# Kernel tuning notes

Hardware: AMD Instinct MI355X
Metric: run time of the kernel (lower is better)

## Reference

```python
import jax, jax.numpy as jnp
import numpy as np

D = 1024
H = 16
DH = D // H
FF = 4096
EPS = 1e-6


def setup_inputs() -> dict:
    key = jax.random.key(0)
    ks = jax.random.split(key, 8)
    s = 1.0 / np.sqrt(D)
    return {
        "x": jax.random.normal(ks[0], (2, 2048, D), jnp.float32),
        # attention projections stored [in, out] (math equals torch Linear x @ W.T)
        "w_q": jax.random.normal(ks[1], (D, D), jnp.float32) * s,
        "w_k": jax.random.normal(ks[2], (D, D), jnp.float32) * s,
        "w_v": jax.random.normal(ks[3], (D, D), jnp.float32) * s,
        "w_o": jax.random.normal(ks[4], (D, D), jnp.float32) * s,
        "w1": jax.random.normal(ks[5], (D, FF), jnp.float32) * s,
        "b1": jnp.zeros((FF,), jnp.float32),
        "w2": jax.random.normal(ks[6], (FF, D), jnp.float32) * (1.0 / np.sqrt(FF)),
        "b2": jnp.zeros((D,), jnp.float32),
        "g1": jnp.ones((D,), jnp.float32),
        "be1": jnp.zeros((D,), jnp.float32),
        "g2": jnp.ones((D,), jnp.float32),
        "be2": jnp.zeros((D,), jnp.float32),
    }


def _layernorm(x, gamma, beta):
    # torch .std() uses Bessel correction (ddof=1); note std+eps, not var+eps
    mean = jnp.mean(x, axis=-1, keepdims=True)
    std = jnp.std(x, axis=-1, keepdims=True, ddof=1)
    return gamma * (x - mean) / (std + EPS) + beta


def _attention(h, w_q, w_k, w_v, w_o):
    B, S, _ = h.shape
    q = (h @ w_q).reshape(B, S, H, DH)
    k = (h @ w_k).reshape(B, S, H, DH)
    v = (h @ w_v).reshape(B, S, H, DH)
    scores = jnp.einsum('bqhd,bkhd->bhqk', q, k) / np.sqrt(DH)  # [B,H,S,S]
    attn = jax.nn.softmax(scores, axis=-1)
    out = jnp.einsum('bhqk,bkhd->bqhd', attn, v).reshape(B, S, D)
    return out @ w_o


def reference(x, w_q, w_k, w_v, w_o, w1, b1, w2, b2, g1, be1, g2, be2):
    # pre-norm residual 1: self-attention (dropout=0 / eval)
    x = x + _attention(_layernorm(x, g1, be1), w_q, w_k, w_v, w_o)
    # pre-norm residual 2: FFN
    h = _layernorm(x, g2, be2)
    x = x + (jax.nn.relu(h @ w1 + b1) @ w2 + b2)
    return x
```

## Files before the change

### kernel.cpp

```cpp
#include <hip/hip_runtime.h>


typedef _Float16 half8 __attribute__((ext_vector_type(8)));
typedef _Float16 half4 __attribute__((ext_vector_type(4)));
typedef float floatx4 __attribute__((ext_vector_type(4)));

__device__ __forceinline__ void async16(const void* g, void* l) {
    __builtin_amdgcn_global_load_lds((const __attribute__((address_space(1))) unsigned int*)g,
                                     (__attribute__((address_space(3))) unsigned int*)l,
                                     16, 0, 0);
}

__global__ __launch_bounds__(256) void ln_kernel(const float* __restrict__ x,
                                                 const float* __restrict__ g,
                                                 const float* __restrict__ be,
                                                 _Float16* __restrict__ out) {
    int row = blockIdx.x;
    int tid = threadIdx.x;
    floatx4 v = ((const floatx4*)(x + (size_t)row * 1024))[tid];
    float s = 0.f, ss = 0.f;
#pragma unroll
    for (int i = 0; i < 4; i++) { s += v[i]; ss += v[i] * v[i]; }
#pragma unroll
    for (int off = 1; off < 64; off <<= 1) {
        s += __shfl_xor(s, off);
        ss += __shfl_xor(ss, off);
    }
    __shared__ float sm[8];
    int wave = tid >> 6, lane = tid & 63;
    if (lane == 0) { sm[wave] = s; sm[wave + 4] = ss; }
    __syncthreads();
    s = sm[0] + sm[1] + sm[2] + sm[3];
    ss = sm[4] + sm[5] + sm[6] + sm[7];
    float mean = s * (1.f / 1024.f);
    float var = (ss - s * mean) * (1.f / 1023.f);
    float rs = 1.f / (sqrtf(fmaxf(var, 0.f)) + 1e-6f);
    floatx4 gv = ((const floatx4*)g)[tid];
    floatx4 bv = ((const floatx4*)be)[tid];
    half4 o;
#pragma unroll
    for (int i = 0; i < 4; i++) o[i] = (_Float16)(gv[i] * (v[i] - mean) * rs + bv[i]);
    ((half4*)(out + (size_t)row * 1024))[tid] = o;
}

__global__ __launch_bounds__(256) void convt_kernel(const float* __restrict__ W, int ldW,
                                                    _Float16* __restrict__ WT, int Kr) {
    __shared__ float t[64][65];
    int n0 = blockIdx.x * 64, k0 = blockIdx.y * 64;
    int tid = threadIdx.x;
    int r = tid >> 4, c4 = (tid & 15) * 4;
#pragma unroll
    for (int p = 0; p < 4; p++) {
        floatx4 v = *(const floatx4*)(W + (size_t)(k0 + r + p * 16) * ldW + n0 + c4);
#pragma unroll
        for (int j = 0; j < 4; j++) t[c4 + j][r + p * 16] = v[j];
    }
    __syncthreads();
#pragma unroll
    for (int p = 0; p < 4; p++) {
        int rr = r + p * 16;
        half4 o;
#pragma unroll
        for (int j = 0; j < 4; j++) o[j] = (_Float16)t[rr][c4 + j];
        *(half4*)(WT + (size_t)(n0 + rr) * Kr + k0 + c4) = o;
    }
}

__global__ __launch_bounds__(256) void transv_kernel(const _Float16* __restrict__ V,
                                                     _Float16* __restrict__ Vt) {
    __shared__ _Float16 t[64][72];
    int t0 = blockIdx.x * 64, d0 = blockIdx.y * 64;
    int tid = threadIdx.x;
#pragma unroll
    for (int i = 0; i < 2; i++) {
        int v = tid + i * 256;
        int r = v >> 3, c = (v & 7) * 8;
        half8 vv = *(const half8*)(V + (size_t)(t0 + r) * 1024 + d0 + c);
#pragma unroll
        for (int j = 0; j < 8; j++) t[c + j][r] = vv[j];
    }
    __syncthreads();
    int bh = (t0 >> 11) * 16 + (d0 >> 6);
    int sbase = t0 & 2047;
#pragma unroll
    for (int i = 0; i < 2; i++) {
        int v = tid + i * 256;
        int r = v >> 3, c = (v & 7) * 8;
        half8 o = *(const half8*)&t[r][c];
        *(half8*)(Vt + ((size_t)bh * 64 + r) * 2048 + sbase + c) = o;
    }
}

__global__ __launch_bounds__(256) void gemm_t(const _Float16* __restrict__ A,
                                              const _Float16* __restrict__ BT,
                                              const float* __restrict__ bias,
                                              const float* res, void* Cout,
                                              int N, int K, int relu_flag, int out_fp16) {
    __shared__ _Float16 As[64 * 64];
    __shared__ _Float16 Bs[128 * 64];
    int tid = threadIdx.x;
    int wave = tid >> 6, lane = tid & 63, quad = lane >> 4, l15 = lane & 15;
    int bm = blockIdx.y * 64, bn = blockIdx.x * 128;
    int wr = (wave & 1) * 32, wc = (wave >> 1) * 64;
    int lrow = lane >> 3, lch = lane & 7;

    floatx4 acc[2][4];
#pragma unroll
    for (int im = 0; im < 2; im++)
#pragma unroll
        for (int in = 0; in < 4; in++)
#pragma unroll
            for (int r = 0; r < 4; r++) acc[im][in][r] = 0.f;

    for (int k0 = 0; k0 < K; k0 += 64) {
        __syncthreads();
#pragma unroll
        for (int ia = 0; ia < 2; ia++) {
            int gidx = 2 * wave + ia;
            int row = gidx * 8 + lrow;
            int ch = lch ^ (row & 7);
            async16(A + (size_t)(bm + row) * K + k0 + ch * 8, &As[gidx * 512]);
        }
#pragma unroll
        for (int ib = 0; ib < 4; ib++) {
            int gidx = 4 * wave + ib;
            int row = gidx * 8 + lrow;
            int ch = lch ^ (row & 7);
            async16(BT + (size_t)(bn + row) * K + k0 + ch * 8, &Bs[gidx * 512]);
        }
        __syncthreads();

        half8 af[2][2], bf[4][2];
#pragma unroll
        for (int kk = 0; kk < 2; kk++) {
#pragma unroll
            for (int im = 0; im < 2; im++) {
                int m = wr + im * 16 + l15;
                af[im][kk] = *(const half8*)&As[m * 64 + ((((kk << 2) | quad) ^ (m & 7)) << 3)];
            }
#pragma unroll
            for (int in = 0; in < 4; in++) {
                int n = wc + in * 16 + l15;
                bf[in][kk] = *(const half8*)&Bs[n * 64 + ((((kk << 2) | quad) ^ (n & 7)) << 3)];
            }
        }
#pragma unroll
        for (int kk = 0; kk < 2; kk++)
#pragma unroll
            for (int im = 0; im < 2; im++)
#pragma unroll
                for (int in = 0; in < 4; in++)
                    acc[im][in] = __builtin_amdgcn_mfma_f32_16x16x32_f16(af[im][kk], bf[in][kk],
                                                                         acc[im][in], 0, 0, 0);
    }
#pragma unroll
    for (int im = 0; im < 2; im++)
#pragma unroll
        for (int in = 0; in < 4; in++)
#pragma unroll
            for (int r = 0; r < 4; r++) {
                int row = bm + wr + im * 16 + quad * 4 + r;
                int col = bn + wc + in * 16 + l15;
                float val = acc[im][in][r];
                if (bias) val += bias[col];
                if (relu_flag) val = fmaxf(val, 0.f);
                if (res) val += res[(size_t)row * N + col];
                if (out_fp16) ((_Float16*)Cout)[(size_t)row * N + col] = (_Float16)val;
                else          ((float*)Cout)[(size_t)row * N + col] = val;
            }
}

__global__ __launch_bounds__(256) void attn_kernel(const _Float16* Q,
                                                   const _Float16* __restrict__ K,
                                                   const _Float16* __restrict__ Vt,
                                                   _Float16* O) {
    __shared__ _Float16 Qs[64 * 64];
    __shared__ _Float16 Ks[64 * 64];
    __shared__ _Float16 Vs[64 * 64];
    int qt = blockIdx.x, bh = blockIdx.y;
    int b = bh >> 4, h = bh & 15;
    int col0 = h * 64, tbase = b * 2048;
    int tid = threadIdx.x;
    int wave = tid >> 6, lane = tid & 63, quad = lane >> 4, l15 = lane & 15;
    int lrow = lane >> 3, lch = lane & 7;

#pragma unroll
    for (int i = 0; i < 2; i++) {
        int g = 2 * wave + i;
        int row = g * 8 + lrow;
        int ch = lch ^ (row & 7);
        async16(Q + (size_t)(tbase + qt * 64 + row) * 1024 + col0 + ch * 8, &Qs[g * 512]);
    }

    floatx4 o_acc[4];
#pragma unroll
    for (int im = 0; im < 4; im++)
#pragma unroll
        for (int r = 0; r < 4; r++) o_acc[im][r] = 0.f;
    float m_i = -1e30f, l_i = 0.f;

    for (int kt = 0; kt < 32; kt++) {
        __syncthreads();
#pragma unroll
        for (int i = 0; i < 2; i++) {
            int g = 2 * wave + i;
            int row = g * 8 + lrow;
            int ch = lch ^ (row & 7);
            async16(K + (size_t)(tbase + kt * 64 + row) * 1024 + col0 + ch * 8, &Ks[g * 512]);
            async16(Vt + ((size_t)bh * 64 + row) * 2048 + kt * 64 + ch * 8, &Vs[g * 512]);
        }
        __syncthreads();

        int rowq = 16 * wave + l15;
        half8 bq[2];
#pragma unroll
        for (int kk = 0; kk < 2; kk++)
            bq[kk] = *(const half8*)&Qs[rowq * 64 + ((((kk << 2) | quad) ^ (rowq & 7)) << 3)];
        floatx4 s_acc[4];
#pragma unroll
        for (int jn = 0; jn < 4; jn++)
#pragma unroll
            for (int r = 0; r < 4; r++) s_acc[jn][r] = 0.f;
#pragma unroll
        for (int jn = 0; jn < 4; jn++) {
            int rowk = 16 * jn + l15;
#pragma unroll
            for (int kk = 0; kk < 2; kk++) {
                half8 ak = *(const half8*)&Ks[rowk * 64 + ((((kk << 2) | quad) ^ (rowk & 7)) << 3)];
                s_acc[jn] = __builtin_amdgcn_mfma_f32_16x16x32_f16(ak, bq[kk], s_acc[jn], 0, 0, 0);
            }
        }

        float mx = -1e30f;
#pragma unroll
        for (int jn = 0; jn < 4; jn++)
#pragma unroll
            for (int r = 0; r < 4; r++) {
                s_acc[jn][r] *= 0.125f;
                mx = fmaxf(mx, s_acc[jn][r]);
            }
        mx = fmaxf(mx, __shfl_xor(mx, 16));
        mx = fmaxf(mx, __shfl_xor(mx, 32));
        float mnew = fmaxf(m_i, mx);
        float dd = m_i - mnew;
        float alpha = (dd < -60.f) ? 0.f : __expf(dd);
        m_i = mnew;

        float sum = 0.f;
#pragma unroll
        for (int jn = 0; jn < 4; jn++)
#pragma unroll
            for (int r = 0; r < 4; r++) {
                float d2 = s_acc[jn][r] - mnew;
                float p = (d2 < -60.f) ? 0.f : __expf(d2);
                s_acc[jn][r] = p;
                sum += p;
            }
        sum += __shfl_xor(sum, 16);
        sum += __shfl_xor(sum, 32);
        l_i = l_i * alpha + sum;

        half4 pb[4];
#pragma unroll
        for (int jn = 0; jn < 4; jn++)
#pragma unroll
            for (int r = 0; r < 4; r++) pb[jn][r] = (_Float16)s_acc[jn][r];

#pragma unroll
        for (int im = 0; im < 4; im++)
#pragma unroll
            for (int r = 0; r < 4; r++) o_acc[im][r] *= alpha;
#pragma unroll
        for (int im = 0; im < 4; im++) {
            int rowv = 16 * im + l15;
#pragma unroll
            for (int ks = 0; ks < 4; ks++) {
                int off = rowv * 128 + ((((2 * ks) | (quad >> 1)) ^ (rowv & 7)) << 4) + (quad & 1) * 8;
                half4 av = *(const half4*)((const char*)Vs + off);
                o_acc[im] = __builtin_amdgcn_mfma_f32_16x16x16f16(av, pb[ks], o_acc[im], 0, 0, 0);
            }
        }
    }

    float rl = 1.f / l_i;
#pragma unroll
    for (int im = 0; im < 4; im++) {
        half4 o;
#pragma unroll
        for (int r = 0; r < 4; r++) o[r] = (_Float16)(o_acc[im][r] * rl);
        *(half4*)&O[(size_t)(tbase + qt * 64 + wave * 16 + l15) * 1024 + col0 + im * 16 + quad * 4] = o;
    }
}

extern "C" void kernel_launch(void* const* d_in, const int* in_sizes, int n_in,
                              void* d_out, int out_size, void* d_ws, size_t ws_size,
                              hipStream_t stream) {
    const float* x   = (const float*)d_in[0];
    const float* wq  = (const float*)d_in[1];
    const float* wk  = (const float*)d_in[2];
    const float* wv  = (const float*)d_in[3];
    const float* wo  = (const float*)d_in[4];
    const float* w1  = (const float*)d_in[5];
    const float* b1  = (const float*)d_in[6];
    const float* w2  = (const float*)d_in[7];
    const float* b2  = (const float*)d_in[8];
    const float* g1  = (const float*)d_in[9];
    const float* be1 = (const float*)d_in[10];
    const float* g2  = (const float*)d_in[11];
    const float* be2 = (const float*)d_in[12];

    const size_t M1 = (size_t)1 << 20;
    _Float16* R0 = (_Float16*)d_ws;
    _Float16* R1 = R0 + 4 * M1;
    _Float16* R2 = R0 + 8 * M1;
    _Float16* R3 = R0 + 12 * M1;

    _Float16* wqT = (_Float16*)d_out;
    _Float16* wkT = wqT + 1 * M1;
    _Float16* wvT = wqT + 2 * M1;
    float* x1 = (float*)d_out;
    float* out = (float*)d_out;

    dim3 blk(256);

    convt_kernel<<<dim3(16, 16), blk, 0, stream>>>(wq, 1024, wqT, 1024);
    convt_kernel<<<dim3(16, 16), blk, 0, stream>>>(wk, 1024, wkT, 1024);
    convt_kernel<<<dim3(16, 16), blk, 0, stream>>>(wv, 1024, wvT, 1024);
    ln_kernel<<<4096, blk, 0, stream>>>(x, g1, be1, R0);
    gemm_t<<<dim3(8, 64), blk, 0, stream>>>(R0, wqT, nullptr, nullptr, R1, 1024, 1024, 0, 1);
    gemm_t<<<dim3(8, 64), blk, 0, stream>>>(R0, wkT, nullptr, nullptr, R2, 1024, 1024, 0, 1);
    gemm_t<<<dim3(8, 64), blk, 0, stream>>>(R0, wvT, nullptr, nullptr, R3, 1024, 1024, 0, 1);
    transv_kernel<<<dim3(64, 16), blk, 0, stream>>>(R3, R0);
    attn_kernel<<<dim3(32, 32), blk, 0, stream>>>(R1, R2, R0, R1);
    convt_kernel<<<dim3(16, 16), blk, 0, stream>>>(wo, 1024, R3, 1024);
    gemm_t<<<dim3(8, 64), blk, 0, stream>>>(R1, R3, nullptr, x, x1, 1024, 1024, 0, 0);
    ln_kernel<<<4096, blk, 0, stream>>>(x1, g2, be2, R0);
    for (int hh = 0; hh < 2; hh++) {
        _Float16* w1Th = R3;
        _Float16* w2Th = R3 + 2 * M1;
        convt_kernel<<<dim3(32, 16), blk, 0, stream>>>(w1 + hh * 2048, 4096, w1Th, 1024);
        gemm_t<<<dim3(16, 64), blk, 0, stream>>>(R0, w1Th, b1 + hh * 2048, nullptr, R1,
                                                 2048, 1024, 1, 1);
        convt_kernel<<<dim3(16, 32), blk, 0, stream>>>(w2 + (size_t)hh * 2048 * 1024, 1024, w2Th, 2048);
        gemm_t<<<dim3(8, 64), blk, 0, stream>>>(R1, w2Th, (hh == 1) ? b2 : nullptr, x1, out,
                                                1024, 2048, 0, 0);
    }
}
```

Baseline: 461.1 us.

## Fuse QKV projections into one GEMM and enlarge GEMM tile to 128x128

The three Q/K/V projection GEMMs become a single GEMM with N=3072 against a concatenated transposed weight. The output is an interleaved QKV buffer, and the attention and V-transpose kernels now take a row stride to read it. The GEMM block tile grows from 64x128 to 128x128, so each wave computes 64x64 with 16 accumulators, which raises operand reuse per LDS load. The cost is more registers and LDS per block and fewer blocks in flight (e.g. 256 blocks for the N=1024 GEMMs), which may leave CUs underused on this large GPU.

After: 522.3 us. 13.3% more time.

```diff
diff --git a/kernel.cpp b/kernel.cpp
--- a/kernel.cpp
+++ b/kernel.cpp
@@ -66,7 +66,7 @@
     }
 }
 
-__global__ __launch_bounds__(256) void transv_kernel(const _Float16* __restrict__ V,
+__global__ __launch_bounds__(256) void transv_kernel(const _Float16* __restrict__ V, int ldv,
                                                      _Float16* __restrict__ Vt) {
     __shared__ _Float16 t[64][72];
     int t0 = blockIdx.x * 64, d0 = blockIdx.y * 64;
@@ -75,7 +75,7 @@
     for (int i = 0; i < 2; i++) {
         int v = tid + i * 256;
         int r = v >> 3, c = (v & 7) * 8;
-        half8 vv = *(const half8*)(V + (size_t)(t0 + r) * 1024 + d0 + c);
+        half8 vv = *(const half8*)(V + (size_t)(t0 + r) * ldv + d0 + c);
 #pragma unroll
         for (int j = 0; j < 8; j++) t[c + j][r] = vv[j];
     }
@@ -91,22 +91,22 @@
     }
 }
 
-__global__ __launch_bounds__(256) void gemm_t(const _Float16* __restrict__ A,
+__global__ __launch_bounds__(256) void gemm_t(const _Float16* __restrict__ A, int lda,
                                               const _Float16* __restrict__ BT,
                                               const float* __restrict__ bias,
                                               const float* res, void* Cout,
                                               int N, int K, int relu_flag, int out_fp16) {
-    __shared__ _Float16 As[64 * 64];
+    __shared__ _Float16 As[128 * 64];
     __shared__ _Float16 Bs[128 * 64];
     int tid = threadIdx.x;
     int wave = tid >> 6, lane = tid & 63, quad = lane >> 4, l15 = lane & 15;
-    int bm = blockIdx.y * 64, bn = blockIdx.x * 128;
-    int wr = (wave & 1) * 32, wc = (wave >> 1) * 64;
+    int bm = blockIdx.y * 128, bn = blockIdx.x * 128;
+    int wm = (wave >> 1) * 64, wn = (wave & 1) * 64;
     int lrow = lane >> 3, lch = lane & 7;
 
-    floatx4 acc[2][4];
-#pragma unroll
-    for (int im = 0; im < 2; im++)
+    floatx4 acc[4][4];
+#pragma unroll
+    for (int im = 0; im < 4; im++)
 #pragma unroll
         for (int in = 0; in < 4; in++)
 #pragma unroll
@@ -115,52 +115,52 @@
     for (int k0 = 0; k0 < K; k0 += 64) {
         __syncthreads();
 #pragma unroll
-        for (int ia = 0; ia < 2; ia++) {
-            int gidx = 2 * wave + ia;
-            int row = gidx * 8 + lrow;
+        for (int ia = 0; ia < 4; ia++) {
+            int g = 4 * wave + ia;
+            int row = g * 8 + lrow;
             int ch = lch ^ (row & 7);
-            async16(A + (size_t)(bm + row) * K + k0 + ch * 8, &As[gidx * 512]);
+            async16(A + (size_t)(bm + row) * lda + k0 + ch * 8, &As[g * 512]);
         }
 #pragma unroll
         for (int ib = 0; ib < 4; ib++) {
-            int gidx = 4 * wave + ib;
-            int row = gidx * 8 + lrow;
+            int g = 4 * wave + ib;
+            int row = g * 8 + lrow;
             int ch = lch ^ (row & 7);
-            async16(BT + (size_t)(bn + row) * K + k0 + ch * 8, &Bs[gidx * 512]);
+            async16(BT + (size_t)(bn + row) * K + k0 + ch * 8, &Bs[g * 512]);
         }
         __syncthreads();
 
-        half8 af[2][2], bf[4][2];
+        half8 af[4][2], bf[4][2];
 #pragma unroll
         for (int kk = 0; kk < 2; kk++) {
 #pragma unroll
-            for (int im = 0; im < 2; im++) {
-                int m = wr + im * 16 + l15;
+            for (int im = 0; im < 4; im++) {
+                int m = wm + im * 16 + l15;
                 af[im][kk] = *(const half8*)&As[m * 64 + ((((kk << 2) | quad) ^ (m & 7)) << 3)];
             }
 #pragma unroll
             for (int in = 0; in < 4; in++) {
-                int n = wc + in * 16 + l15;
+                int n = wn + in * 16 + l15;
                 bf[in][kk] = *(const half8*)&Bs[n * 64 + ((((kk << 2) | quad) ^ (n & 7)) << 3)];
             }
         }
 #pragma unroll
         for (int kk = 0; kk < 2; kk++)
 #pragma unroll
-            for (int im = 0; im < 2; im++)
+            for (int im = 0; im < 4; im++)
 #pragma unroll
                 for (int in = 0; in < 4; in++)
                     acc[im][in] = __builtin_amdgcn_mfma_f32_16x16x32_f16(af[im][kk], bf[in][kk],
                                                                          acc[im][in], 0, 0, 0);
     }
 #pragma unroll
-    for (int im = 0; im < 2; im++)
+    for (int im = 0; im < 4; im++)
 #pragma unroll
         for (int in = 0; in < 4; in++)
 #pragma unroll
             for (int r = 0; r < 4; r++) {
-                int row = bm + wr + im * 16 + quad * 4 + r;
-                int col = bn + wc + in * 16 + l15;
+                int row = bm + wm + im * 16 + quad * 4 + r;
+                int col = bn + wn + in * 16 + l15;
                 float val = acc[im][in][r];
                 if (bias) val += bias[col];
                 if (relu_flag) val = fmaxf(val, 0.f);
@@ -173,7 +173,7 @@
 __global__ __launch_bounds__(256) void attn_kernel(const _Float16* Q,
                                                    const _Float16* __restrict__ K,
                                                    const _Float16* __restrict__ Vt,
-                                                   _Float16* O) {
+                                                   _Float16* O, int ld) {
     __shared__ _Float16 Qs[64 * 64];
     __shared__ _Float16 Ks[64 * 64];
     __shared__ _Float16 Vs[64 * 64];
@@ -189,7 +189,7 @@
         int g = 2 * wave + i;
         int row = g * 8 + lrow;
         int ch = lch ^ (row & 7);
-        async16(Q + (size_t)(tbase + qt * 64 + row) * 1024 + col0 + ch * 8, &Qs[g * 512]);
+        async16(Q + (size_t)(tbase + qt * 64 + row) * ld + col0 + ch * 8, &Qs[g * 512]);
     }
 
     floatx4 o_acc[4];
@@ -206,7 +206,7 @@
             int g = 2 * wave + i;
             int row = g * 8 + lrow;
             int ch = lch ^ (row & 7);
-            async16(K + (size_t)(tbase + kt * 64 + row) * 1024 + col0 + ch * 8, &Ks[g * 512]);
+            async16(K + (size_t)(tbase + kt * 64 + row) * ld + col0 + ch * 8, &Ks[g * 512]);
             async16(Vt + ((size_t)bh * 64 + row) * 2048 + kt * 64 + ch * 8, &Vs[g * 512]);
         }
         __syncthreads();
@@ -288,7 +288,7 @@
         half4 o;
 #pragma unroll
         for (int r = 0; r < 4; r++) o[r] = (_Float16)(o_acc[im][r] * rl);
-        *(half4*)&O[(size_t)(tbase + qt * 64 + wave * 16 + l15) * 1024 + col0 + im * 16 + quad * 4] = o;
+        *(half4*)&O[(size_t)(tbase + qt * 64 + wave * 16 + l15) * ld + col0 + im * 16 + quad * 4] = o;
     }
 }
 
@@ -310,39 +310,35 @@
     const float* be2 = (const float*)d_in[12];
 
     const size_t M1 = (size_t)1 << 20;
-    _Float16* R0 = (_Float16*)d_ws;
-    _Float16* R1 = R0 + 4 * M1;
-    _Float16* R2 = R0 + 8 * M1;
-    _Float16* R3 = R0 + 12 * M1;
-
-    _Float16* wqT = (_Float16*)d_out;
-    _Float16* wkT = wqT + 1 * M1;
-    _Float16* wvT = wqT + 2 * M1;
+    _Float16* R0  = (_Float16*)d_ws;
+    _Float16* QKV = R0 + 4 * M1;
+    _Float16* R3  = R0 + 12 * M1;
+
+    _Float16* wqkvT = (_Float16*)d_out;
     float* x1 = (float*)d_out;
     float* out = (float*)d_out;
 
     dim3 blk(256);
 
-    convt_kernel<<<dim3(16, 16), blk, 0, stream>>>(wq, 1024, wqT, 1024);
-    convt_kernel<<<dim3(16, 16), blk, 0, stream>>>(wk, 1024, wkT, 1024);
-    convt_kernel<<<dim3(16, 16), blk, 0, stream>>>(wv, 1024, wvT, 1024);
+    convt_kernel<<<dim3(16, 16), blk, 0, stream>>>(wq, 1024, wqkvT, 1024);
+    convt_kernel<<<dim3(16, 16), blk, 0, stream>>>(wk, 1024, wqkvT + (size_t)1024 * 1024, 1024);
+    convt_kernel<<<dim3(16, 16), blk, 0, stream>>>(wv, 1024, wqkvT + (size_t)2048 * 1024, 1024);
     ln_kernel<<<4096, blk, 0, stream>>>(x, g1, be1, R0);
-    gemm_t<<<dim3(8, 64), blk, 0, stream>>>(R0, wqT, nullptr, nullptr, R1, 1024, 1024, 0, 1);
-    gemm_t<<<dim3(8, 64), blk, 0, stream>>>(R0, wkT, nullptr, nullptr, R2, 1024, 1024, 0, 1);
-    gemm_t<<<dim3(8, 64), blk, 0, stream>>>(R0, wvT, nullptr, nullptr, R3, 1024, 1024, 0, 1);
-    transv_kernel<<<dim3(64, 16), blk, 0, stream>>>(R3, R0);
-    attn_kernel<<<dim3(32, 32), blk, 0, stream>>>(R1, R2, R0, R1);
-    convt_kernel<<<dim3(16, 16), blk, 0, stream>>>(wo, 1024, R3, 1024);
-    gemm_t<<<dim3(8, 64), blk, 0, stream>>>(R1, R3, nullptr, x, x1, 1024, 1024, 0, 0);
+    gemm_t<<<dim3(24, 32), blk, 0, stream>>>(R0, 1024, wqkvT, nullptr, nullptr, QKV, 3072, 1024, 0, 1);
+    transv_kernel<<<dim3(64, 16), blk, 0, stream>>>(QKV + 2048, 3072, R0);
+    attn_kernel<<<dim3(32, 32), blk, 0, stream>>>(QKV, QKV + 1024, R0, QKV, 3072);
+    convt_kernel<<<dim3(16, 16), blk, 0, stream>>>(wo, 1024, R0, 1024);
+    gemm_t<<<dim3(8, 32), blk, 0, stream>>>(QKV, 3072, R0, nullptr, x, x1, 1024, 1024, 0, 0);
     ln_kernel<<<4096, blk, 0, stream>>>(x1, g2, be2, R0);
+    _Float16* f = QKV;
     for (int hh = 0; hh < 2; hh++) {
         _Float16* w1Th = R3;
         _Float16* w2Th = R3 + 2 * M1;
         convt_kernel<<<dim3(32, 16), blk, 0, stream>>>(w1 + hh * 2048, 4096, w1Th, 1024);
-        gemm_t<<<dim3(16, 64), blk, 0, stream>>>(R0, w1Th, b1 + hh * 2048, nullptr, R1,
+        gemm_t<<<dim3(16, 32), blk, 0, stream>>>(R0, 1024, w1Th, b1 + hh * 2048, nullptr, f,
                                                  2048, 1024, 1, 1);
         convt_kernel<<<dim3(16, 32), blk, 0, stream>>>(w2 + (size_t)hh * 2048 * 1024, 1024, w2Th, 2048);
-        gemm_t<<<dim3(8, 64), blk, 0, stream>>>(R1, w2Th, (hh == 1) ? b2 : nullptr, x1, out,
+        gemm_t<<<dim3(8, 32), blk, 0, stream>>>(f, 2048, w2Th, (hh == 1) ? b2 : nullptr, x1, out,
                                                 1024, 2048, 0, 0);
     }
 }
```
